# Kernel optimization log

Measured on AMD Instinct MI355X. Metric: run time of the kernel, lower is better.

The kernel has to match this reference:

```python
import jax, jax.numpy as jnp
import numpy as np

B, S, D, H = 2, 2048, 1024, 16
HD = D // H

def setup_inputs() -> dict:
    key = jax.random.key(0)
    ks = jax.random.split(key, 12)
    std = 1.0 / np.sqrt(D)
    query = jax.random.normal(ks[0], (B, S, D), jnp.float32)
    kk = jax.random.normal(ks[1], (B, S, D), jnp.float32)
    vv = jax.random.normal(ks[2], (B, S, D), jnp.float32)
    # per-batch valid lengths; True = padded position
    lengths = jax.random.randint(ks[3], (B,), S // 2, S + 1)
    key_padding_mask = jnp.arange(S)[None, :] >= lengths[:, None]
    Wq = jax.random.uniform(ks[4], (D, D), jnp.float32, -std, std)
    bq = jnp.zeros((D,), jnp.float32)
    Wk = jax.random.uniform(ks[5], (D, D), jnp.float32, -std, std)
    bk = jnp.zeros((D,), jnp.float32)
    Wv = jax.random.uniform(ks[6], (D, D), jnp.float32, -std, std)
    bv = jnp.zeros((D,), jnp.float32)
    Wo = jax.random.uniform(ks[7], (D, D), jnp.float32, -std, std)
    bo = jnp.zeros((D,), jnp.float32)
    return {"query": query, "key": kk, "value": vv,
            "key_padding_mask": key_padding_mask,
            "Wq": Wq, "bq": bq, "Wk": Wk, "bk": bk,
            "Wv": Wv, "bv": bv, "Wo": Wo, "bo": bo}

def reference(query, key, value, key_padding_mask, Wq, bq, Wk, bk, Wv, bv, Wo, bo):
    scale = HD ** -0.5
    # projections -> [B, H, S, HD]
    def proj(x, W, b):
        return (x @ W.T + b).reshape(B, S, H, HD).transpose(0, 2, 1, 3)
    q = proj(query, Wq, bq)
    k = proj(key, Wk, bk)
    v = proj(value, Wv, bv)
    scores = jnp.einsum('bhqd,bhkd->bhqk', q, k) * scale  # [B,H,S,S]
    pos = jnp.arange(S)
    rel_bias = -0.1 * jnp.abs(pos[:, None] - pos[None, :]).astype(scores.dtype)
    scores = scores + rel_bias[None, None]
    scores = jnp.where(key_padding_mask[:, None, None, :], -jnp.inf, scores)
    attn = jax.nn.softmax(scores, axis=-1)  # dropout is identity in eval
    out = jnp.einsum('bhqk,bhkd->bhqd', attn, v)
    out = out.transpose(0, 2, 1, 3).reshape(B, S, D)
    return out @ Wo.T + bo
```

## Files before the change

kernel.cpp:

```cpp
#include <hip/hip_runtime.h>

typedef __attribute__((ext_vector_type(8))) short bf16x8;
typedef __attribute__((ext_vector_type(4))) short s16x4;
typedef __attribute__((ext_vector_type(8))) short s16x8;
typedef __attribute__((ext_vector_type(4))) float fx4;

static __device__ __forceinline__ short f2bf(float f) {
  unsigned u = __builtin_bit_cast(unsigned, f);
  u += 0x7fffu + ((u >> 16) & 1u);
  return (short)(u >> 16);
}

static __device__ __forceinline__ void gload_lds16(const void* g, void* l) {
  __builtin_amdgcn_global_load_lds(
      (const __attribute__((address_space(1))) unsigned int*)g,
      (__attribute__((address_space(3))) unsigned int*)l, 16, 0, 0);
}

#define BB_ 2
#define SS_ 2048
#define DD_ 1024
#define HH_ 16
#define HD_ 64

__global__ __launch_bounds__(256) void cvt_kernel(
    const float* __restrict__ q, const float* __restrict__ k, const float* __restrict__ v,
    const float* __restrict__ Wq, const float* __restrict__ Wk, const float* __restrict__ Wv,
    const float* __restrict__ Wo,
    short* __restrict__ xq, short* __restrict__ xk, short* __restrict__ xv,
    short* __restrict__ wq, short* __restrict__ wk, short* __restrict__ wv,
    short* __restrict__ wo) {
  size_t e = ((size_t)blockIdx.x * 256 + threadIdx.x) * 8;
  const float* src; short* dst; size_t off;
  if (e < 4194304u)        { src = q;  dst = xq; off = e; }
  else if (e < 8388608u)   { src = k;  dst = xk; off = e - 4194304u; }
  else if (e < 12582912u)  { src = v;  dst = xv; off = e - 8388608u; }
  else if (e < 13631488u)  { src = Wq; dst = wq; off = e - 12582912u; }
  else if (e < 14680064u)  { src = Wk; dst = wk; off = e - 13631488u; }
  else if (e < 15728640u)  { src = Wv; dst = wv; off = e - 14680064u; }
  else                     { src = Wo; dst = wo; off = e - 15728640u; }
  fx4 a = *(const fx4*)(src + off);
  fx4 b = *(const fx4*)(src + off + 4);
  s16x8 o;
  o[0] = f2bf(a[0]); o[1] = f2bf(a[1]); o[2] = f2bf(a[2]); o[3] = f2bf(a[3]);
  o[4] = f2bf(b[0]); o[5] = f2bf(b[1]); o[6] = f2bf(b[2]); o[7] = f2bf(b[3]);
  *(s16x8*)(dst + off) = o;
}

__global__ __launch_bounds__(256) void proj_gemm(
    const short* __restrict__ xq, const short* __restrict__ xk, const short* __restrict__ xv,
    const short* __restrict__ wq, const short* __restrict__ wk, const short* __restrict__ wv,
    const float* __restrict__ bq, const float* __restrict__ bk, const float* __restrict__ bv,
    short* __restrict__ qout, short* __restrict__ kout, short* __restrict__ vtout) {
  constexpr int K = DD_;
  __shared__ short As[128 * 32];
  __shared__ short Bs[128 * 32];
  int z = blockIdx.z;
  const short* A = (z == 0) ? xq : ((z == 1) ? xk : xv);
  const short* W = (z == 0) ? wq : ((z == 1) ? wk : wv);
  const float* bias = (z == 0) ? bq : ((z == 1) ? bk : bv);
  int m0 = blockIdx.x * 128, n0 = blockIdx.y * 128;
  int tid = threadIdx.x, lane = tid & 63, wv_ = tid >> 6;
  int wr = wv_ >> 1, wc = wv_ & 1;
  int c = lane & 15, g = lane >> 4;
  fx4 acc[4][4] = {};

  const char* Ab = (const char*)A;
  const char* Wb = (const char*)W;
  for (int k0 = 0; k0 < K; k0 += 32) {
    __syncthreads();
#pragma unroll
    for (int cc = 0; cc < 2; cc++) {
      int o = (cc * 256 + tid) * 16;
      int row = o >> 6, colb = o & 63;
      gload_lds16(Ab + ((size_t)(m0 + row) * K + k0) * 2 + colb, ((char*)As) + o);
      gload_lds16(Wb + ((size_t)(n0 + row) * K + k0) * 2 + colb, ((char*)Bs) + o);
    }
    __syncthreads();
    bf16x8 a[4], b[4];
#pragma unroll
    for (int i = 0; i < 4; i++) a[i] = *(const bf16x8*)(As + (wr * 64 + i * 16 + c) * 32 + g * 8);
#pragma unroll
    for (int j = 0; j < 4; j++) b[j] = *(const bf16x8*)(Bs + (wc * 64 + j * 16 + c) * 32 + g * 8);
#pragma unroll
    for (int i = 0; i < 4; i++)
#pragma unroll
      for (int j = 0; j < 4; j++)
        acc[i][j] = __builtin_amdgcn_mfma_f32_16x16x32_bf16(a[i], b[j], acc[i][j], 0, 0, 0);
  }

#pragma unroll
  for (int i = 0; i < 4; i++)
#pragma unroll
    for (int j = 0; j < 4; j++) {
      int gcol = n0 + wc * 64 + j * 16 + c;
      float bv_ = bias[gcol];
      int hh = gcol >> 6, hd = gcol & 63;
      if (z == 2) {
        int grow0 = m0 + wr * 64 + i * 16 + g * 4;
        int bb = grow0 >> 11, s0 = grow0 & 2047;
        s16x4 pk;
#pragma unroll
        for (int r = 0; r < 4; r++) pk[r] = f2bf(acc[i][j][r] + bv_);
        *(s16x4*)(vtout + ((size_t)((bb * HH_ + hh) * HD_ + hd) * SS_ + s0)) = pk;
      } else {
#pragma unroll
        for (int r = 0; r < 4; r++) {
          int grow = m0 + wr * 64 + i * 16 + g * 4 + r;
          int bb = grow >> 11, s = grow & 2047;
          float val = acc[i][j][r] + bv_;
          size_t idx = ((size_t)(bb * HH_ + hh) * SS_ + s) * HD_ + hd;
          if (z == 0) qout[idx] = f2bf(val * 0.125f);
          else        kout[idx] = f2bf(val);
        }
      }
    }
}

__global__ __launch_bounds__(256) void attn_kernel(
    const short* __restrict__ qb, const short* __restrict__ kb, const short* __restrict__ vt,
    const int* __restrict__ mask, short* __restrict__ aout) {
  __shared__ float mb2[SS_];
  __shared__ char Ksh[2][8192];
  __shared__ char Vsh[2][8192];
  __shared__ char Plds[4][2048];

  int L = blockIdx.x;
  int W = (L & 7) * 128 + (L >> 3);
  int qblk = W & 31, h = (W >> 5) & 15, b = W >> 9;

  int tid = threadIdx.x, lane = tid & 63, w = tid >> 6;
  int c = lane & 15, g = lane >> 4;
  for (int i = tid; i < SS_; i += 256) mb2[i] = mask[b * SS_ + i] ? -1e30f : 0.0f;

  const char* Kp = (const char*)(kb + (size_t)(b * HH_ + h) * SS_ * HD_);
  const char* Vp = (const char*)(vt + (size_t)(b * HH_ + h) * HD_ * SS_);

  int r8 = lane >> 3, c8 = lane & 7;
  int swz = (c8 ^ r8) * 16;
  int iA = w * 2, iB = w * 2 + 1;
  int kOffA = (iA * 8 + r8) * 128 + swz;
  int kOffB = (iB * 8 + r8) * 128 + swz;
  int vOffA = (iA * 8 + r8) * 4096 + swz;
  int vOffB = (iB * 8 + r8) * 4096 + swz;

  gload_lds16(Kp + kOffA, &Ksh[0][iA * 1024]);
  gload_lds16(Kp + kOffB, &Ksh[0][iB * 1024]);
  gload_lds16(Vp + vOffA, &Vsh[0][iA * 1024]);
  gload_lds16(Vp + vOffB, &Vsh[0][iB * 1024]);
  __syncthreads();

  int nt = 1;
  while (nt < 32 && mb2[nt * 64] > -1e29f) nt++;

  int q0 = qblk * 64 + w * 16;
  const short* Qp = qb + (size_t)(b * HH_ + h) * SS_ * HD_;
  bf16x8 aq0 = *(const bf16x8*)(Qp + (q0 + c) * HD_ + g * 8);
  bf16x8 aq1 = *(const bf16x8*)(Qp + (q0 + c) * HD_ + 32 + g * 8);
  fx4 o[4] = {};
  float m_run = -1e30f, l_run = 0.0f;
  float qf = (float)(q0 + c);
  char* Pw = Plds[w];
  const float L2E = 1.44269504f;
  int cs = c & 7;
  int rc0 = (g ^ cs) * 16;
  int rc1 = ((4 + g) ^ cs) * 16;

  for (int t = 0; t < nt; ++t) {
    int cur = t & 1;
    if (t + 1 < nt) {
      const char* kpp = Kp + (t + 1) * 64 * 128;
      const char* vpp = Vp + (t + 1) * 64 * 2;
      gload_lds16(kpp + kOffA, &Ksh[cur ^ 1][iA * 1024]);
      gload_lds16(kpp + kOffB, &Ksh[cur ^ 1][iB * 1024]);
      gload_lds16(vpp + vOffA, &Vsh[cur ^ 1][iA * 1024]);
      gload_lds16(vpp + vOffB, &Vsh[cur ^ 1][iB * 1024]);
    }
    int kv0 = t * 64;
    const char* Kc = Ksh[cur];
    const char* Vc = Vsh[cur];

    fx4 s[4];
    __builtin_amdgcn_s_setprio(1);
#pragma unroll
    for (int tt = 0; tt < 4; tt++) {
      bf16x8 ak0 = *(const bf16x8*)(Kc + (tt * 16 + c) * 128 + rc0);
      bf16x8 ak1 = *(const bf16x8*)(Kc + (tt * 16 + c) * 128 + rc1);
      fx4 z4 = {};
      s[tt] = __builtin_amdgcn_mfma_f32_16x16x32_bf16(ak0, aq0, z4, 0, 0, 0);
      s[tt] = __builtin_amdgcn_mfma_f32_16x16x32_bf16(ak1, aq1, s[tt], 0, 0, 0);
    }
    __builtin_amdgcn_s_setprio(0);

    float p[16];
    float tmax = -3e38f;
#pragma unroll
    for (int tt = 0; tt < 4; tt++) {
      fx4 mbv = *(const fx4*)&mb2[kv0 + tt * 16 + g * 4];
#pragma unroll
      for (int r = 0; r < 4; r++) {
        float kvf = (float)(kv0 + tt * 16 + g * 4 + r);
        float s2 = fmaf(s[tt][r], L2E, fmaf(-0.1f * L2E, fabsf(qf - kvf), mbv[r]));
        p[tt * 4 + r] = s2;
        tmax = fmaxf(tmax, s2);
      }
    }
    tmax = fmaxf(tmax, __shfl_xor(tmax, 16));
    tmax = fmaxf(tmax, __shfl_xor(tmax, 32));
    float m_new = fmaxf(m_run, tmax);
    float fsc = __builtin_amdgcn_exp2f(m_run - m_new);
    m_run = m_new;
    float psum = 0.f;
#pragma unroll
    for (int i = 0; i < 16; i++) {
      p[i] = __builtin_amdgcn_exp2f(p[i] - m_new);
      psum += p[i];
    }
    psum += __shfl_xor(psum, 16);
    psum += __shfl_xor(psum, 32);
    l_run = l_run * fsc + psum;

#pragma unroll
    for (int tt = 0; tt < 4; tt++) {
      s16x4 pk;
      pk[0] = f2bf(p[tt * 4 + 0]); pk[1] = f2bf(p[tt * 4 + 1]);
      pk[2] = f2bf(p[tt * 4 + 2]); pk[3] = f2bf(p[tt * 4 + 3]);
      *(s16x4*)(Pw + c * 128 + ((2 * tt + (g >> 1)) ^ cs) * 16 + (g & 1) * 8) = pk;
    }
#pragma unroll
    for (int r = 0; r < 4; r++) {
      float fr = __shfl(fsc, g * 4 + r);
      o[0][r] *= fr; o[1][r] *= fr; o[2][r] *= fr; o[3][r] *= fr;
    }
    bf16x8 pa0 = *(const bf16x8*)(Pw + c * 128 + rc0);
    bf16x8 pa1 = *(const bf16x8*)(Pw + c * 128 + rc1);
    __builtin_amdgcn_s_setprio(1);
#pragma unroll
    for (int n = 0; n < 4; n++) {
      bf16x8 v0 = *(const bf16x8*)(Vc + (n * 16 + c) * 128 + rc0);
      bf16x8 v1 = *(const bf16x8*)(Vc + (n * 16 + c) * 128 + rc1);
      o[n] = __builtin_amdgcn_mfma_f32_16x16x32_bf16(pa0, v0, o[n], 0, 0, 0);
      o[n] = __builtin_amdgcn_mfma_f32_16x16x32_bf16(pa1, v1, o[n], 0, 0, 0);
    }
    __builtin_amdgcn_s_setprio(0);

    __syncthreads();
  }

  float linv[4];
#pragma unroll
  for (int r = 0; r < 4; r++) linv[r] = 1.0f / __shfl(l_run, g * 4 + r);
#pragma unroll
  for (int n = 0; n < 4; n++)
#pragma unroll
    for (int r = 0; r < 4; r++) {
      int qrow = q0 + g * 4 + r;
      float val = o[n][r] * linv[r];
      aout[((size_t)(b * SS_ + qrow)) * DD_ + h * HD_ + n * 16 + c] = f2bf(val);
    }
}

__global__ __launch_bounds__(256) void oproj_gemm(
    const short* __restrict__ A, const short* __restrict__ W,
    const float* __restrict__ bias, float* __restrict__ out) {
  constexpr int K = DD_;
  __shared__ short As[128 * 32];
  __shared__ short Bs[128 * 32];
  int m0 = blockIdx.x * 128, n0 = blockIdx.y * 128;
  int tid = threadIdx.x, lane = tid & 63, wv_ = tid >> 6;
  int wr = wv_ >> 1, wc = wv_ & 1;
  int c = lane & 15, g = lane >> 4;
  fx4 acc[4][4] = {};
  const char* Ab = (const char*)A;
  const char* Wb = (const char*)W;
  for (int k0 = 0; k0 < K; k0 += 32) {
    __syncthreads();
#pragma unroll
    for (int cc = 0; cc < 2; cc++) {
      int o = (cc * 256 + tid) * 16;
      int row = o >> 6, colb = o & 63;
      gload_lds16(Ab + ((size_t)(m0 + row) * K + k0) * 2 + colb, ((char*)As) + o);
      gload_lds16(Wb + ((size_t)(n0 + row) * K + k0) * 2 + colb, ((char*)Bs) + o);
    }
    __syncthreads();
    bf16x8 a[4], b[4];
#pragma unroll
    for (int i = 0; i < 4; i++) a[i] = *(const bf16x8*)(As + (wr * 64 + i * 16 + c) * 32 + g * 8);
#pragma unroll
    for (int j = 0; j < 4; j++) b[j] = *(const bf16x8*)(Bs + (wc * 64 + j * 16 + c) * 32 + g * 8);
#pragma unroll
    for (int i = 0; i < 4; i++)
#pragma unroll
      for (int j = 0; j < 4; j++)
        acc[i][j] = __builtin_amdgcn_mfma_f32_16x16x32_bf16(a[i], b[j], acc[i][j], 0, 0, 0);
  }
#pragma unroll
  for (int i = 0; i < 4; i++)
#pragma unroll
    for (int j = 0; j < 4; j++) {
      int gcol = n0 + wc * 64 + j * 16 + c;
      float bv_ = bias[gcol];
#pragma unroll
      for (int r = 0; r < 4; r++) {
        int grow = m0 + wr * 64 + i * 16 + g * 4 + r;
        out[(size_t)grow * DD_ + gcol] = acc[i][j][r] + bv_;
      }
    }
}

extern "C" void kernel_launch(void* const* d_in, const int* in_sizes, int n_in,
                              void* d_out, int out_size, void* d_ws, size_t ws_size,
                              hipStream_t stream) {
  const float* q  = (const float*)d_in[0];
  const float* k  = (const float*)d_in[1];
  const float* v  = (const float*)d_in[2];
  const int* mask = (const int*)d_in[3];
  const float* Wq = (const float*)d_in[4];
  const float* bq = (const float*)d_in[5];
  const float* Wk = (const float*)d_in[6];
  const float* bk = (const float*)d_in[7];
  const float* Wv = (const float*)d_in[8];
  const float* bv = (const float*)d_in[9];
  const float* Wo = (const float*)d_in[10];
  const float* bo = (const float*)d_in[11];

  char* ws = (char*)d_ws;
  short* qbuf = (short*)(ws);
  short* kbuf = (short*)(ws + (8ull << 20));
  short* vtb  = (short*)(ws + (16ull << 20));
  short* abuf = (short*)(ws + (24ull << 20));
  short* xq   = (short*)(ws + (32ull << 20));
  short* xk   = (short*)(ws + (40ull << 20));
  short* xv   = (short*)(ws + (48ull << 20));
  short* wq   = (short*)(ws + (56ull << 20));
  short* wk   = (short*)(ws + (58ull << 20));
  short* wv   = (short*)(ws + (60ull << 20));
  short* wo   = (short*)(ws + (62ull << 20));
  float* out  = (float*)d_out;

  cvt_kernel<<<8192, 256, 0, stream>>>(q, k, v, Wq, Wk, Wv, Wo, xq, xk, xv, wq, wk, wv, wo);
  dim3 gp(32, 8, 3);
  proj_gemm<<<gp, 256, 0, stream>>>(xq, xk, xv, wq, wk, wv, bq, bk, bv, qbuf, kbuf, vtb);
  attn_kernel<<<1024, 256, 0, stream>>>(qbuf, kbuf, vtb, mask, abuf);
  dim3 go(32, 8, 1);
  oproj_gemm<<<go, 256, 0, stream>>>(abuf, wo, bo, out);
}
```

Baseline: 273.5 us.

## Double-buffer GEMMs with 512 threads and streamline attention masking and rescale

Both projection GEMMs move to 512-thread blocks with double-buffered LDS tiles, so the next K-slice loads while MFMAs run on the current one, and there is one barrier per iteration instead of two. The attention kernel drops the per-block mask table in LDS. It instead computes the valid length with a wave reduction and masks only the last tile. It also skips the online-softmax rescale of the accumulators unless the running max grows by more than a threshold. The lazy rescale relies on bounded exp2 growth, and the length derivation assumes the mask is a contiguous padding suffix.

```diff
diff --git a/kernel.cpp b/kernel.cpp
--- a/kernel.cpp
+++ b/kernel.cpp
@@ -47,69 +47,75 @@
   *(s16x8*)(dst + off) = o;
 }
 
-__global__ __launch_bounds__(256) void proj_gemm(
+__global__ __launch_bounds__(512) void proj_gemm(
     const short* __restrict__ xq, const short* __restrict__ xk, const short* __restrict__ xv,
     const short* __restrict__ wq, const short* __restrict__ wk, const short* __restrict__ wv,
     const float* __restrict__ bq, const float* __restrict__ bk, const float* __restrict__ bv,
     short* __restrict__ qout, short* __restrict__ kout, short* __restrict__ vtout) {
   constexpr int K = DD_;
-  __shared__ short As[128 * 32];
-  __shared__ short Bs[128 * 32];
+  __shared__ short As[2][128 * 32];
+  __shared__ short Bs[2][128 * 32];
   int z = blockIdx.z;
   const short* A = (z == 0) ? xq : ((z == 1) ? xk : xv);
   const short* W = (z == 0) ? wq : ((z == 1) ? wk : wv);
   const float* bias = (z == 0) ? bq : ((z == 1) ? bk : bv);
   int m0 = blockIdx.x * 128, n0 = blockIdx.y * 128;
   int tid = threadIdx.x, lane = tid & 63, wv_ = tid >> 6;
-  int wr = wv_ >> 1, wc = wv_ & 1;
+  int wr = wv_ >> 2, wc = wv_ & 3;
   int c = lane & 15, g = lane >> 4;
-  fx4 acc[4][4] = {};
-
-  const char* Ab = (const char*)A;
-  const char* Wb = (const char*)W;
+  fx4 acc[4][2] = {};
+
+  const char* Ab = (const char*)A + (size_t)m0 * K * 2;
+  const char* Wb = (const char*)W + (size_t)n0 * K * 2;
+  int o = tid * 16;
+  int row = o >> 6, colb = o & 63;
+  size_t aoff = (size_t)row * (K * 2) + colb;
+
+  gload_lds16(Ab + aoff, ((char*)As[0]) + o);
+  gload_lds16(Wb + aoff, ((char*)Bs[0]) + o);
+  __syncthreads();
+
   for (int k0 = 0; k0 < K; k0 += 32) {
+    int cur = (k0 >> 5) & 1;
+    if (k0 + 32 < K) {
+      size_t off = aoff + (size_t)(k0 + 32) * 2;
+      gload_lds16(Ab + off, ((char*)As[cur ^ 1]) + o);
+      gload_lds16(Wb + off, ((char*)Bs[cur ^ 1]) + o);
+    }
+    bf16x8 a[4], bb[2];
+#pragma unroll
+    for (int i = 0; i < 4; i++) a[i] = *(const bf16x8*)(As[cur] + (wr * 64 + i * 16 + c) * 32 + g * 8);
+#pragma unroll
+    for (int j = 0; j < 2; j++) bb[j] = *(const bf16x8*)(Bs[cur] + (wc * 32 + j * 16 + c) * 32 + g * 8);
+#pragma unroll
+    for (int i = 0; i < 4; i++)
+#pragma unroll
+      for (int j = 0; j < 2; j++)
+        acc[i][j] = __builtin_amdgcn_mfma_f32_16x16x32_bf16(a[i], bb[j], acc[i][j], 0, 0, 0);
     __syncthreads();
-#pragma unroll
-    for (int cc = 0; cc < 2; cc++) {
-      int o = (cc * 256 + tid) * 16;
-      int row = o >> 6, colb = o & 63;
-      gload_lds16(Ab + ((size_t)(m0 + row) * K + k0) * 2 + colb, ((char*)As) + o);
-      gload_lds16(Wb + ((size_t)(n0 + row) * K + k0) * 2 + colb, ((char*)Bs) + o);
-    }
-    __syncthreads();
-    bf16x8 a[4], b[4];
-#pragma unroll
-    for (int i = 0; i < 4; i++) a[i] = *(const bf16x8*)(As + (wr * 64 + i * 16 + c) * 32 + g * 8);
-#pragma unroll
-    for (int j = 0; j < 4; j++) b[j] = *(const bf16x8*)(Bs + (wc * 64 + j * 16 + c) * 32 + g * 8);
-#pragma unroll
-    for (int i = 0; i < 4; i++)
-#pragma unroll
-      for (int j = 0; j < 4; j++)
-        acc[i][j] = __builtin_amdgcn_mfma_f32_16x16x32_bf16(a[i], b[j], acc[i][j], 0, 0, 0);
   }
 
 #pragma unroll
   for (int i = 0; i < 4; i++)
 #pragma unroll
-    for (int j = 0; j < 4; j++) {
-      int gcol = n0 + wc * 64 + j * 16 + c;
+    for (int j = 0; j < 2; j++) {
+      int gcol = n0 + wc * 32 + j * 16 + c;
       float bv_ = bias[gcol];
       int hh = gcol >> 6, hd = gcol & 63;
       if (z == 2) {
         int grow0 = m0 + wr * 64 + i * 16 + g * 4;
-        int bb = grow0 >> 11, s0 = grow0 & 2047;
+        int bb2 = grow0 >> 11, s0 = grow0 & 2047;
         s16x4 pk;
 #pragma unroll
         for (int r = 0; r < 4; r++) pk[r] = f2bf(acc[i][j][r] + bv_);
-        *(s16x4*)(vtout + ((size_t)((bb * HH_ + hh) * HD_ + hd) * SS_ + s0)) = pk;
+        *(s16x4*)(vtout + ((size_t)((bb2 * HH_ + hh) * HD_ + hd) * SS_ + s0)) = pk;
       } else {
 #pragma unroll
         for (int r = 0; r < 4; r++) {
           int grow = m0 + wr * 64 + i * 16 + g * 4 + r;
-          int bb = grow >> 11, s = grow & 2047;
+          int bb2 = grow >> 11, s = grow & 2047;
           float val = acc[i][j][r] + bv_;
-          size_t idx = ((size_t)(bb * HH_ + hh) * SS_ + s) * HD_ + hd;
+          size_t idx = ((size_t)(bb2 * HH_ + hh) * SS_ + s) * HD_ + hd;
           if (z == 0) qout[idx] = f2bf(val * 0.125f);
           else        kout[idx] = f2bf(val);
         }
@@ -120,7 +126,6 @@
 __global__ __launch_bounds__(256) void attn_kernel(
     const short* __restrict__ qb, const short* __restrict__ kb, const short* __restrict__ vt,
     const int* __restrict__ mask, short* __restrict__ aout) {
-  __shared__ float mb2[SS_];
   __shared__ char Ksh[2][8192];
   __shared__ char Vsh[2][8192];
   __shared__ char Plds[4][2048];
@@ -131,7 +136,6 @@
 
   int tid = threadIdx.x, lane = tid & 63, w = tid >> 6;
   int c = lane & 15, g = lane >> 4;
-  for (int i = tid; i < SS_; i += 256) mb2[i] = mask[b * SS_ + i] ? -1e30f : 0.0f;
 
   const char* Kp = (const char*)(kb + (size_t)(b * HH_ + h) * SS_ * HD_);
   const char* Vp = (const char*)(vt + (size_t)(b * HH_ + h) * HD_ * SS_);
@@ -148,10 +152,20 @@
   gload_lds16(Kp + kOffB, &Ksh[0][iB * 1024]);
   gload_lds16(Vp + vOffA, &Vsh[0][iA * 1024]);
   gload_lds16(Vp + vOffB, &Vsh[0][iB * 1024]);
+
+  int lmin = SS_;
+  for (int i = lane; i < SS_; i += 64)
+    if (mask[b * SS_ + i] && i < lmin) lmin = i;
+#pragma unroll
+  for (int off = 32; off >= 1; off >>= 1) {
+    int o2 = __shfl_xor(lmin, off);
+    lmin = (o2 < lmin) ? o2 : lmin;
+  }
+  int len = lmin;
+  int nt = (len + 63) >> 6;
+  float lenf = (float)len;
+
   __syncthreads();
-
-  int nt = 1;
-  while (nt < 32 && mb2[nt * 64] > -1e29f) nt++;
 
   int q0 = qblk * 64 + w * 16;
   const short* Qp = qb + (size_t)(b * HH_ + h) * SS_ * HD_;
@@ -162,6 +176,7 @@
   float qf = (float)(q0 + c);
   char* Pw = Plds[w];
   const float L2E = 1.44269504f;
+  const float NB = -0.144269504f;
   int cs = c & 7;
   int rc0 = (g ^ cs) * 16;
   int rc1 = ((4 + g) ^ cs) * 16;
@@ -169,14 +184,13 @@
   for (int t = 0; t < nt; ++t) {
     int cur = t & 1;
     if (t + 1 < nt) {
-      const char* kpp = Kp + (t + 1) * 64 * 128;
-      const char* vpp = Vp + (t + 1) * 64 * 2;
+      const char* kpp = Kp + (t + 1) * 8192;
+      const char* vpp = Vp + (t + 1) * 128;
       gload_lds16(kpp + kOffA, &Ksh[cur ^ 1][iA * 1024]);
       gload_lds16(kpp + kOffB, &Ksh[cur ^ 1][iB * 1024]);
       gload_lds16(vpp + vOffA, &Vsh[cur ^ 1][iA * 1024]);
       gload_lds16(vpp + vOffB, &Vsh[cur ^ 1][iB * 1024]);
     }
-    int kv0 = t * 64;
     const char* Kc = Ksh[cur];
     const char* Vc = Vsh[cur];
 
@@ -193,32 +207,51 @@
     __builtin_amdgcn_s_setprio(0);
 
     float p[16];
-    float tmax = -3e38f;
-#pragma unroll
-    for (int tt = 0; tt < 4; tt++) {
-      fx4 mbv = *(const fx4*)&mb2[kv0 + tt * 16 + g * 4];
+    float kvb = (float)(t * 64 + g * 4);
+#pragma unroll
+    for (int tt = 0; tt < 4; tt++)
 #pragma unroll
       for (int r = 0; r < 4; r++) {
-        float kvf = (float)(kv0 + tt * 16 + g * 4 + r);
-        float s2 = fmaf(s[tt][r], L2E, fmaf(-0.1f * L2E, fabsf(qf - kvf), mbv[r]));
-        p[tt * 4 + r] = s2;
-        tmax = fmaxf(tmax, s2);
+        float kvf = kvb + (float)(tt * 16 + r);
+        p[tt * 4 + r] = fmaf(s[tt][r], L2E, NB * fabsf(qf - kvf));
       }
-    }
+    if (t == nt - 1) {
+#pragma unroll
+      for (int tt = 0; tt < 4; tt++)
+#pragma unroll
+        for (int r = 0; r < 4; r++) {
+          float kvf = kvb + (float)(tt * 16 + r);
+          if (kvf >= lenf) p[tt * 4 + r] = -1e30f;
+        }
+    }
+
+    float t0 = fmaxf(fmaxf(p[0], p[1]), fmaxf(p[2], p[3]));
+    float t1 = fmaxf(fmaxf(p[4], p[5]), fmaxf(p[6], p[7]));
+    float t2 = fmaxf(fmaxf(p[8], p[9]), fmaxf(p[10], p[11]));
+    float t3 = fmaxf(fmaxf(p[12], p[13]), fmaxf(p[14], p[15]));
+    float tmax = fmaxf(fmaxf(t0, t1), fmaxf(t2, t3));
     tmax = fmaxf(tmax, __shfl_xor(tmax, 16));
     tmax = fmaxf(tmax, __shfl_xor(tmax, 32));
     float m_new = fmaxf(m_run, tmax);
-    float fsc = __builtin_amdgcn_exp2f(m_run - m_new);
-    m_run = m_new;
+    if (!__all(m_new - m_run <= 8.0f)) {
+      float fsc = __builtin_amdgcn_exp2f(m_run - m_new);
+      m_run = m_new;
+      l_run *= fsc;
+#pragma unroll
+      for (int r = 0; r < 4; r++) {
+        float fr = __shfl(fsc, g * 4 + r);
+        o[0][r] *= fr; o[1][r] *= fr; o[2][r] *= fr; o[3][r] *= fr;
+      }
+    }
     float psum = 0.f;
 #pragma unroll
     for (int i = 0; i < 16; i++) {
-      p[i] = __builtin_amdgcn_exp2f(p[i] - m_new);
+      p[i] = __builtin_amdgcn_exp2f(p[i] - m_run);
       psum += p[i];
     }
     psum += __shfl_xor(psum, 16);
     psum += __shfl_xor(psum, 32);
-    l_run = l_run * fsc + psum;
+    l_run += psum;
 
 #pragma unroll
     for (int tt = 0; tt < 4; tt++) {
@@ -227,11 +260,6 @@
       pk[2] = f2bf(p[tt * 4 + 2]); pk[3] = f2bf(p[tt * 4 + 3]);
       *(s16x4*)(Pw + c * 128 + ((2 * tt + (g >> 1)) ^ cs) * 16 + (g & 1) * 8) = pk;
     }
-#pragma unroll
-    for (int r = 0; r < 4; r++) {
-      float fr = __shfl(fsc, g * 4 + r);
-      o[0][r] *= fr; o[1][r] *= fr; o[2][r] *= fr; o[3][r] *= fr;
-    }
     bf16x8 pa0 = *(const bf16x8*)(Pw + c * 128 + rc0);
     bf16x8 pa1 = *(const bf16x8*)(Pw + c * 128 + rc1);
     __builtin_amdgcn_s_setprio(1);
@@ -260,45 +288,51 @@
     }
 }
 
-__global__ __launch_bounds__(256) void oproj_gemm(
+__global__ __launch_bounds__(512) void oproj_gemm(
     const short* __restrict__ A, const short* __restrict__ W,
     const float* __restrict__ bias, float* __restrict__ out) {
   constexpr int K = DD_;
-  __shared__ short As[128 * 32];
-  __shared__ short Bs[128 * 32];
+  __shared__ short As[2][128 * 32];
+  __shared__ short Bs[2][128 * 32];
   int m0 = blockIdx.x * 128, n0 = blockIdx.y * 128;
   int tid = threadIdx.x, lane = tid & 63, wv_ = tid >> 6;
-  int wr = wv_ >> 1, wc = wv_ & 1;
+  int wr = wv_ >> 2, wc = wv_ & 3;
   int c = lane & 15, g = lane >> 4;
-  fx4 acc[4][4] = {};
-  const char* Ab = (const char*)A;
-  const char* Wb = (const char*)W;
+  fx4 acc[4][2] = {};
+  const char* Ab = (const char*)A + (size_t)m0 * K * 2;
+  const char* Wb = (const char*)W + (size_t)n0 * K * 2;
+  int o = tid * 16;
+  size_t aoff = (size_t)(o >> 6) * (K * 2) + (o & 63);
+
+  gload_lds16(Ab + aoff, ((char*)As[0]) + o);
+  gload_lds16(Wb + aoff, ((char*)Bs[0]) + o);
+  __syncthreads();
+
   for (int k0 = 0; k0 < K; k0 += 32) {
+    int cur = (k0 >> 5) & 1;
+    if (k0 + 32 < K) {
+      size_t off = aoff + (size_t)(k0 + 32) * 2;
+      gload_lds16(Ab + off, ((char*)As[cur ^ 1]) + o);
+      gload_lds16(Wb + off, ((char*)Bs[cur ^ 1]) + o);
+    }
+    bf16x8 a[4], bb[2];
+#pragma unroll
+    for (int i = 0; i < 4; i++) a[i] = *(const bf16x8*)(As[cur] + (wr * 64 + i * 16 + c) * 32 + g * 8);
+#pragma unroll
+    for (int j = 0; j < 2; j++) bb[j] = *(const bf16x8*)(Bs[cur] + (wc * 32 + j * 16 + c) * 32 + g * 8);
+#pragma unroll
+    for (int i = 0; i < 4; i++)
+#pragma unroll
+      for (int j = 0; j < 2; j++)
+        acc[i][j] = __builtin_amdgcn_mfma_f32_16x16x32_bf16(a[i], bb[j], acc[i][j], 0, 0, 0);
     __syncthreads();
-#pragma unroll
-    for (int cc = 0; cc < 2; cc++) {
-      int o = (cc * 256 + tid) * 16;
-      int row = o >> 6, colb = o & 63;
-      gload_lds16(Ab + ((size_t)(m0 + row) * K + k0) * 2 + colb, ((char*)As) + o);
-      gload_lds16(Wb + ((size_t)(n0 + row) * K + k0) * 2 + colb, ((char*)Bs) + o);
-    }
-    __syncthreads();
-    bf16x8 a[4], b[4];
-#pragma unroll
-    for (int i = 0; i < 4; i++) a[i] = *(const bf16x8*)(As + (wr * 64 + i * 16 + c) * 32 + g * 8);
-#pragma unroll
-    for (int j = 0; j < 4; j++) b[j] = *(const bf16x8*)(Bs + (wc * 64 + j * 16 + c) * 32 + g * 8);
-#pragma unroll
-    for (int i = 0; i < 4; i++)
-#pragma unroll
-      for (int j = 0; j < 4; j++)
-        acc[i][j] = __builtin_amdgcn_mfma_f32_16x16x32_bf16(a[i], b[j], acc[i][j], 0, 0, 0);
   }
+
 #pragma unroll
   for (int i = 0; i < 4; i++)
 #pragma unroll
-    for (int j = 0; j < 4; j++) {
-      int gcol = n0 + wc * 64 + j * 16 + c;
+    for (int j = 0; j < 2; j++) {
+      int gcol = n0 + wc * 32 + j * 16 + c;
       float bv_ = bias[gcol];
 #pragma unroll
       for (int r = 0; r < 4; r++) {
@@ -340,8 +374,8 @@
 
   cvt_kernel<<<8192, 256, 0, stream>>>(q, k, v, Wq, Wk, Wv, Wo, xq, xk, xv, wq, wk, wv, wo);
   dim3 gp(32, 8, 3);
-  proj_gemm<<<gp, 256, 0, stream>>>(xq, xk, xv, wq, wk, wv, bq, bk, bv, qbuf, kbuf, vtb);
+  proj_gemm<<<gp, 512, 0, stream>>>(xq, xk, xv, wq, wk, wv, bq, bk, bv, qbuf, kbuf, vtb);
   attn_kernel<<<1024, 256, 0, stream>>>(qbuf, kbuf, vtb, mask, abuf);
   dim3 go(32, 8, 1);
-  oproj_gemm<<<go, 256, 0, stream>>>(abuf, wo, bo, out);
-}
+  oproj_gemm<<<go, 512, 0, stream>>>(abuf, wo, bo, out);
+}
```

Measured after the change: 254.6 us. 1.07x faster.
